# Performance work log

Hardware: AMD Instinct MI355X
Metric: run time of the kernel (lower is better)

Reference implementation:

```python
import jax, jax.numpy as jnp
import numpy as np

EMBED = 1024

def setup_inputs() -> dict:
    key = jax.random.key(0)
    ks = jax.random.split(key, 7)
    s = 1.0 / np.sqrt(EMBED)  # ~ torch Linear default init scale
    x = jax.random.normal(ks[0], (4, 2048, EMBED), dtype=jnp.float32)
    Wq = jax.random.uniform(ks[1], (EMBED, EMBED), jnp.float32, -s, s)
    bq = jax.random.uniform(ks[2], (EMBED,), jnp.float32, -s, s)
    Wk = jax.random.uniform(ks[3], (EMBED, EMBED), jnp.float32, -s, s)
    bk = jax.random.uniform(ks[4], (EMBED,), jnp.float32, -s, s)
    Wv = jax.random.uniform(ks[5], (EMBED, EMBED), jnp.float32, -s, s)
    bv = jax.random.uniform(ks[6], (EMBED,), jnp.float32, -s, s)
    return {"x": x, "Wq": Wq, "bq": bq, "Wk": Wk, "bk": bk, "Wv": Wv, "bv": bv}

def reference(x, Wq, bq, Wk, bk, Wv, bv):
    # torch nn.Linear: y = x @ W.T + b
    q = jnp.einsum('bse,oe->bso', x, Wq) + bq
    k = jnp.einsum('bse,oe->bso', x, Wk) + bk
    v = jnp.einsum('bse,oe->bso', x, Wv) + bv
    scale = 1.0 / jnp.sqrt(jnp.float32(x.shape[-1]))
    scores = jnp.einsum('bqd,bkd->bqk', q, k) * scale  # [B,S,S]
    weights = jax.nn.softmax(scores, axis=-1)
    return jnp.einsum('bqk,bkd->bqd', weights, v)
```

## Files before the change

kernel.cpp:

```cpp
#include <hip/hip_runtime.h>
#include <stdint.h>

#define B_   4
#define S_   2048
#define E_   1024
#define MQKV (B_ * S_)
#define LDP  2112

typedef __bf16 bf16x8 __attribute__((ext_vector_type(8)));
typedef float f32x4 __attribute__((ext_vector_type(4)));
typedef unsigned short u16;
typedef unsigned int u32;

__device__ __forceinline__ u16 f2bf(float x) {
  union { float f; u32 u; } c; c.f = x;
  u32 r = (c.u + 0x7FFFu + ((c.u >> 16) & 1u)) >> 16;
  return (u16)r;
}
__device__ __forceinline__ float bf2f(u16 h) {
  union { u32 u; float f; } c; c.u = ((u32)h) << 16;
  return c.f;
}

__global__ __launch_bounds__(256) void cvt_f32_bf16(const float* __restrict__ src,
                                                    u16* __restrict__ dst, int n4) {
  int i = blockIdx.x * blockDim.x + threadIdx.x;
  int st = gridDim.x * blockDim.x;
  for (; i < n4; i += st) {
    float4 f = reinterpret_cast<const float4*>(src)[i];
    ushort4 o;
    o.x = f2bf(f.x); o.y = f2bf(f.y); o.z = f2bf(f.z); o.w = f2bf(f.w);
    reinterpret_cast<ushort4*>(dst)[i] = o;
  }
}

__global__ __launch_bounds__(256) void cvt_w3(const float* __restrict__ wq,
                                              const float* __restrict__ wk,
                                              const float* __restrict__ wv,
                                              u16* __restrict__ dst) {
  const int per = E_ * E_ / 4;
  int i = blockIdx.x * blockDim.x + threadIdx.x;
  const int sel = i / per;
  const int r = i - sel * per;
  const float* src = sel == 0 ? wq : (sel == 1 ? wk : wv);
  float4 f = reinterpret_cast<const float4*>(src)[r];
  ushort4 o;
  o.x = f2bf(f.x); o.y = f2bf(f.y); o.z = f2bf(f.z); o.w = f2bf(f.w);
  reinterpret_cast<ushort4*>(dst)[i] = o;
}

#define GLOAD_LDS16(g, l)                                                      \
  __builtin_amdgcn_global_load_lds(                                            \
      (const __attribute__((address_space(1))) u32*)(g),                       \
      (__attribute__((address_space(3))) u32*)(l), 16, 0, 0)

template <int BN, int EPI>
__device__ __forceinline__ void gemm_body(
    const u16* __restrict__ A, const u16* __restrict__ Bt, void* __restrict__ Cv,
    const float* __restrict__ b0, const float* __restrict__ b1,
    int N, int K, float scale,
    long sA, long sB, long sC, long ldA, long ldB, long ldC, int gx, int gy) {
  constexpr int BM = 256;
  constexpr int NR = BN / 64;
  constexpr int L  = 2 + BN / 128;
  constexpr int BSLOT = BN * 32;

  __shared__ alignas(16) u16 lds[4 * BM * 32 + 4 * BSLOT];
  u16* lA = lds;
  u16* lB = lds + 4 * BM * 32;

  const int t = threadIdx.x;
  const int wv = t >> 6;
  const int ln = t & 63;
  const int wm = wv >> 2;
  const int wn = wv & 3;

  const int nwg = gridDim.x;
  int id = blockIdx.x;
  id = (id & 7) * (nwg >> 3) + (id >> 3);
  const int pz = gx * gy;
  const int z = id / pz;
  const int r2 = id - z * pz;
  const int by = r2 / gx;
  const int bx = r2 - by * gx;
  const int bm = by * BM;
  const int bn = bx * BN;

  A += (size_t)z * sA;
  Bt += (size_t)z * sB;

  const int srow = t >> 2;
  const int g0 = (t & 3) ^ ((srow >> 1) & 3);
  const u16* gA0 = A + (size_t)(bm + srow) * ldA + g0 * 8;
  const u16* gA1 = gA0 + (size_t)128 * ldA;
  const u16* gB0 = Bt + (size_t)(bn + srow) * ldB + g0 * 8;
  const u16* gB1 = gB0 + (size_t)128 * ldB;

  auto STAGE = [&](int u) {
    const int s = u & 3;
    const int ko = u * 32;
    GLOAD_LDS16(gA0 + ko, lA + s * 8192 + wv * 512);
    GLOAD_LDS16(gA1 + ko, lA + s * 8192 + 4096 + wv * 512);
    GLOAD_LDS16(gB0 + ko, lB + s * BSLOT + wv * 512);
    if constexpr (BN == 256) GLOAD_LDS16(gB1 + ko, lB + s * BSLOT + 4096 + wv * 512);
  };

  const int lrow = ln & 15;
  const int g = ln >> 4;
  const int aR = wm * 128 + lrow;
  const int aOff = aR * 32 + (g ^ ((aR >> 1) & 3)) * 8;
  const int bR = wn * (BN / 4) + lrow;
  const int bOff = bR * 32 + (g ^ ((bR >> 1) & 3)) * 8;

  f32x4 acc[8][NR] = {};
  const int T = K >> 5;

  bf16x8 afA[8], afB[8], bgA[NR], bgB[NR];

#define RD_A(DST, TILE) do { const u16* _p = lA + ((TILE) & 3) * 8192 + aOff;  \
  _Pragma("unroll") for (int _i = 0; _i < 8; ++_i)                             \
    DST[_i] = *reinterpret_cast<const bf16x8*>(_p + _i * 512); } while (0)
#define RD_B(DST, TILE) do { const u16* _p = lB + ((TILE) & 3) * BSLOT + bOff; \
  _Pragma("unroll") for (int _j = 0; _j < NR; ++_j)                            \
    DST[_j] = *reinterpret_cast<const bf16x8*>(_p + _j * 512); } while (0)
#define DO_MFMA(AF, BG) do { __builtin_amdgcn_s_setprio(1);                    \
  _Pragma("unroll") for (int _i = 0; _i < 8; ++_i)                             \
  _Pragma("unroll") for (int _j = 0; _j < NR; ++_j)                            \
    acc[_i][_j] = __builtin_amdgcn_mfma_f32_16x16x32_bf16(AF[_i], BG[_j],      \
                                                          acc[_i][_j], 0, 0, 0);\
  __builtin_amdgcn_s_setprio(0); } while (0)
#define VM_GATE(COND) do {                                                     \
  if (COND) { asm volatile("s_waitcnt vmcnt(%0)" :: "n"(L) : "memory"); }      \
  else { asm volatile("s_waitcnt vmcnt(0)" ::: "memory"); }                    \
  __builtin_amdgcn_s_barrier(); asm volatile("" ::: "memory"); } while (0)

  STAGE(0); STAGE(1); STAGE(2);
  asm volatile("s_waitcnt vmcnt(%0)" :: "n"(L) : "memory");
  __builtin_amdgcn_s_barrier();
  asm volatile("" ::: "memory");

  if constexpr (NR == 2) { RD_A(afA, 0); RD_B(bgA, 0); }
  else                   { RD_B(bgA, 0); }

  for (int tt = 0; tt < T; tt += 2) {
    if (tt + 3 < T) STAGE(tt + 3);
    if constexpr (NR == 2) { RD_A(afB, tt + 1); RD_B(bgB, tt + 1); DO_MFMA(afA, bgA); }
    else                   { RD_A(afA, tt); RD_B(bgB, tt + 1);     DO_MFMA(afA, bgA); }
    VM_GATE(tt + 3 < T);

    if (tt + 4 < T) STAGE(tt + 4);
    if constexpr (NR == 2) {
      if (tt + 2 < T) { RD_A(afA, tt + 2); RD_B(bgA, tt + 2); }
      DO_MFMA(afB, bgB);
    } else {
      RD_A(afA, tt + 1);
      if (tt + 2 < T) RD_B(bgA, tt + 2);
      DO_MFMA(afA, bgB);
    }
    VM_GATE(tt + 4 < T);
  }
#undef RD_A
#undef RD_B
#undef DO_MFMA
#undef VM_GATE

  const int r0 = (ln >> 4) * 4;
  const int c0 = ln & 15;
#pragma unroll
  for (int i = 0; i < 8; ++i) {
#pragma unroll
    for (int j = 0; j < NR; ++j) {
      const int col = bn + wn * (BN / 4) + j * 16 + c0;
#pragma unroll
      for (int ii = 0; ii < 4; ++ii) {
        const int row = bm + wm * 128 + i * 16 + r0 + ii;
        float v = acc[i][j][ii];
        if constexpr (EPI == 0) {
          const int sel = col >> 10;
          const int cc = col & 1023;
          const float bb = sel == 0 ? b0[cc] : b1[cc];
          ((u16*)Cv)[(size_t)sel * 8388608 + (size_t)row * 1024 + cc] = f2bf(v + bb);
        } else if constexpr (EPI == 1) {
          ((u16*)Cv)[(size_t)z * sC + (size_t)row * ldC + col] = f2bf(v + b0[row]);
        } else if constexpr (EPI == 2) {
          ((u16*)Cv)[(size_t)z * sC + (size_t)row * ldC + col] = f2bf(__expf(v * scale));
        } else {
          ((float*)Cv)[(size_t)z * sC + (size_t)row * ldC + col] = v * b0[z * 2048 + row];
        }
      }
    }
  }
}

__global__ __launch_bounds__(512, 2) void qkproj_k(
    const u16* __restrict__ A, const u16* __restrict__ Bt, void* __restrict__ Cv,
    const float* __restrict__ b0, const float* __restrict__ b1,
    int N, int K, float scale, long sA, long sB, long sC,
    long ldA, long ldB, long ldC, int gx, int gy) {
  gemm_body<256, 0>(A, Bt, Cv, b0, b1, N, K, scale, sA, sB, sC, ldA, ldB, ldC, gx, gy);
}
__global__ __launch_bounds__(512, 2) void vproj_k(
    const u16* __restrict__ A, const u16* __restrict__ Bt, void* __restrict__ Cv,
    const float* __restrict__ b0, const float* __restrict__ b1,
    int N, int K, float scale, long sA, long sB, long sC,
    long ldA, long ldB, long ldC, int gx, int gy) {
  gemm_body<128, 1>(A, Bt, Cv, b0, b1, N, K, scale, sA, sB, sC, ldA, ldB, ldC, gx, gy);
}
__global__ __launch_bounds__(512, 2) void qkt_k(
    const u16* __restrict__ A, const u16* __restrict__ Bt, void* __restrict__ Cv,
    const float* __restrict__ b0, const float* __restrict__ b1,
    int N, int K, float scale, long sA, long sB, long sC,
    long ldA, long ldB, long ldC, int gx, int gy) {
  gemm_body<256, 2>(A, Bt, Cv, b0, b1, N, K, scale, sA, sB, sC, ldA, ldB, ldC, gx, gy);
}
__global__ __launch_bounds__(512, 2) void pv_k(
    const u16* __restrict__ A, const u16* __restrict__ Bt, void* __restrict__ Cv,
    const float* __restrict__ b0, const float* __restrict__ b1,
    int N, int K, float scale, long sA, long sB, long sC,
    long ldA, long ldB, long ldC, int gx, int gy) {
  gemm_body<128, 3>(A, Bt, Cv, b0, b1, N, K, scale, sA, sB, sC, ldA, ldB, ldC, gx, gy);
}

__global__ __launch_bounds__(256) void row_invsum(const u16* __restrict__ P,
                                                  float* __restrict__ invL) {
  const int row = blockIdx.x * 4 + (threadIdx.x >> 6);
  const int ln = threadIdx.x & 63;
  const u16* p = P + (size_t)row * LDP + ln * 32;
  float s = 0.f;
#pragma unroll
  for (int q = 0; q < 4; ++q) {
    uint4 r = reinterpret_cast<const uint4*>(p)[q];
    u32 w[4] = {r.x, r.y, r.z, r.w};
#pragma unroll
    for (int k = 0; k < 4; ++k) {
      s += bf2f((u16)(w[k] & 0xffffu));
      s += bf2f((u16)(w[k] >> 16));
    }
  }
  for (int o = 1; o < 64; o <<= 1) s += __shfl_xor(s, o);
  if (ln == 0) invL[row] = 1.0f / s;
}

extern "C" void kernel_launch(void* const* d_in, const int* in_sizes, int n_in,
                              void* d_out, int out_size, void* d_ws, size_t ws_size,
                              hipStream_t stream) {
  const float* x = (const float*)d_in[0];
  const float* Wq = (const float*)d_in[1];
  const float* bq = (const float*)d_in[2];
  const float* Wk = (const float*)d_in[3];
  const float* bk = (const float*)d_in[4];
  const float* Wv = (const float*)d_in[5];
  const float* bv = (const float*)d_in[6];
  float* out = (float*)d_out;

  const size_t xE = 8388608, wE = 3145728, qE = 8388608;
  const size_t vtE = (size_t)4 * 1024 * LDP;
  const size_t PmE = (size_t)4 * 2048 * LDP;
  const size_t need = (xE + wE + 2 * qE + vtE + PmE) * 2 + (size_t)MQKV * 4;
  if (ws_size < need) {
    hipMemsetAsync(d_out, 0, (size_t)out_size * sizeof(float), stream);
    return;
  }
  u16* xb = (u16*)d_ws;
  u16* wqkv = xb + xE;
  u16* qb = wqkv + wE;
  u16* vt = qb + 2 * qE;
  u16* Pm = vt + vtE;
  float* invL = (float*)(Pm + PmE);

  cvt_f32_bf16<<<2048, 256, 0, stream>>>(x, xb, MQKV * E_ / 4);
  cvt_w3<<<3 * E_ * E_ / 4 / 256, 256, 0, stream>>>(Wq, Wk, Wv, wqkv);

  qkproj_k<<<256, 512, 0, stream>>>(
      xb, wqkv, qb, bq, bk, 2048, E_, 1.f,
      0, 0, 0, E_, E_, 1024, 8, 32);

  vproj_k<<<256, 512, 0, stream>>>(
      wqkv + 2 * (size_t)E_ * E_, xb, vt, bv, nullptr, 2048, E_, 1.f,
      0, (long)S_ * E_, (long)1024 * LDP, E_, E_, LDP, 16, 4);

  qkt_k<<<256, 512, 0, stream>>>(
      qb, qb + 8388608, Pm, nullptr, nullptr, 2048, E_, 0.03125f,
      (long)S_ * 1024, (long)S_ * 1024, (long)2048 * LDP, 1024, 1024, LDP, 8, 8);

  row_invsum<<<B_ * S_ / 4, 256, 0, stream>>>(Pm, invL);

  pv_k<<<256, 512, 0, stream>>>(
      Pm, vt, out, invL, nullptr, E_, S_, 1.f,
      (long)2048 * LDP, (long)1024 * LDP, (long)S_ * E_, LDP, LDP, 1024, 8, 8);
}
```

Baseline: 157.8 us.

## Fuse softmax row sums into QK^T epilogue and add dedicated PV kernel

The QK^T epilogue now accumulates each row's exp sum with shuffles and atomics into a zeroed buffer, which removes the separate row_invsum pass over the probability matrix. The two conversion kernels become one launch that also zeroes that buffer. PV gets its own kernel with a 3-stage LDS pipeline, 64-wide K steps and XOR swizzling, and the normalization is applied in its epilogue. This trades one launch and a full re-read of P for atomic traffic and a new, hand-scheduled GEMM loop.

```diff
diff --git a/kernel.cpp b/kernel.cpp
--- a/kernel.cpp
+++ b/kernel.cpp
@@ -17,36 +17,30 @@
   u32 r = (c.u + 0x7FFFu + ((c.u >> 16) & 1u)) >> 16;
   return (u16)r;
 }
-__device__ __forceinline__ float bf2f(u16 h) {
-  union { u32 u; float f; } c; c.u = ((u32)h) << 16;
-  return c.f;
-}
-
-__global__ __launch_bounds__(256) void cvt_f32_bf16(const float* __restrict__ src,
-                                                    u16* __restrict__ dst, int n4) {
-  int i = blockIdx.x * blockDim.x + threadIdx.x;
-  int st = gridDim.x * blockDim.x;
-  for (; i < n4; i += st) {
-    float4 f = reinterpret_cast<const float4*>(src)[i];
+
+__global__ __launch_bounds__(256) void cvt_all(
+    const float* __restrict__ x, const float* __restrict__ wq,
+    const float* __restrict__ wk, const float* __restrict__ wv,
+    u16* __restrict__ dst, float* __restrict__ Ls) {
+  const int gid = blockIdx.x * 256 + threadIdx.x;
+  if (gid < MQKV) Ls[gid] = 0.f;
+  const int total = 2097152 + 786432;
+  const int stride = gridDim.x * 256;
+  for (int i = gid; i < total; i += stride) {
+    float4 f;
+    if (i < 2097152) {
+      f = reinterpret_cast<const float4*>(x)[i];
+    } else {
+      const int j = i - 2097152;
+      const int sel = j >> 18;
+      const int r = j & 262143;
+      const float* s = sel == 0 ? wq : (sel == 1 ? wk : wv);
+      f = reinterpret_cast<const float4*>(s)[r];
+    }
     ushort4 o;
     o.x = f2bf(f.x); o.y = f2bf(f.y); o.z = f2bf(f.z); o.w = f2bf(f.w);
     reinterpret_cast<ushort4*>(dst)[i] = o;
   }
-}
-
-__global__ __launch_bounds__(256) void cvt_w3(const float* __restrict__ wq,
-                                              const float* __restrict__ wk,
-                                              const float* __restrict__ wv,
-                                              u16* __restrict__ dst) {
-  const int per = E_ * E_ / 4;
-  int i = blockIdx.x * blockDim.x + threadIdx.x;
-  const int sel = i / per;
-  const int r = i - sel * per;
-  const float* src = sel == 0 ? wq : (sel == 1 ? wk : wv);
-  float4 f = reinterpret_cast<const float4*>(src)[r];
-  ushort4 o;
-  o.x = f2bf(f.x); o.y = f2bf(f.y); o.z = f2bf(f.z); o.w = f2bf(f.w);
-  reinterpret_cast<ushort4*>(dst)[i] = o;
 }
 
 #define GLOAD_LDS16(g, l)                                                      \
@@ -57,7 +51,7 @@
 template <int BN, int EPI>
 __device__ __forceinline__ void gemm_body(
     const u16* __restrict__ A, const u16* __restrict__ Bt, void* __restrict__ Cv,
-    const float* __restrict__ b0, const float* __restrict__ b1,
+    const float* __restrict__ b0, const float* __restrict__ b1, float* __restrict__ Ls,
     int N, int K, float scale,
     long sA, long sB, long sC, long ldA, long ldB, long ldC, int gx, int gy) {
   constexpr int BM = 256;
@@ -166,26 +160,43 @@
 
   const int r0 = (ln >> 4) * 4;
   const int c0 = ln & 15;
-#pragma unroll
-  for (int i = 0; i < 8; ++i) {
-#pragma unroll
-    for (int j = 0; j < NR; ++j) {
-      const int col = bn + wn * (BN / 4) + j * 16 + c0;
+  if constexpr (EPI == 2) {
+#pragma unroll
+    for (int i = 0; i < 8; ++i) {
 #pragma unroll
       for (int ii = 0; ii < 4; ++ii) {
         const int row = bm + wm * 128 + i * 16 + r0 + ii;
-        float v = acc[i][j][ii];
-        if constexpr (EPI == 0) {
-          const int sel = col >> 10;
-          const int cc = col & 1023;
-          const float bb = sel == 0 ? b0[cc] : b1[cc];
-          ((u16*)Cv)[(size_t)sel * 8388608 + (size_t)row * 1024 + cc] = f2bf(v + bb);
-        } else if constexpr (EPI == 1) {
-          ((u16*)Cv)[(size_t)z * sC + (size_t)row * ldC + col] = f2bf(v + b0[row]);
-        } else if constexpr (EPI == 2) {
-          ((u16*)Cv)[(size_t)z * sC + (size_t)row * ldC + col] = f2bf(__expf(v * scale));
-        } else {
-          ((float*)Cv)[(size_t)z * sC + (size_t)row * ldC + col] = v * b0[z * 2048 + row];
+        float s = 0.f;
+#pragma unroll
+        for (int j = 0; j < NR; ++j) {
+          const int col = bn + wn * (BN / 4) + j * 16 + c0;
+          const float vex = __expf(acc[i][j][ii] * scale);
+          ((u16*)Cv)[(size_t)z * sC + (size_t)row * ldC + col] = f2bf(vex);
+          s += vex;
+        }
+        s += __shfl_xor(s, 1); s += __shfl_xor(s, 2);
+        s += __shfl_xor(s, 4); s += __shfl_xor(s, 8);
+        if ((ln & 15) == 0) unsafeAtomicAdd(&Ls[z * 2048 + row], s);
+      }
+    }
+  } else {
+#pragma unroll
+    for (int i = 0; i < 8; ++i) {
+#pragma unroll
+      for (int j = 0; j < NR; ++j) {
+        const int col = bn + wn * (BN / 4) + j * 16 + c0;
+#pragma unroll
+        for (int ii = 0; ii < 4; ++ii) {
+          const int row = bm + wm * 128 + i * 16 + r0 + ii;
+          float v = acc[i][j][ii];
+          if constexpr (EPI == 0) {
+            const int sel = col >> 10;
+            const int cc = col & 1023;
+            const float bb = sel == 0 ? b0[cc] : b1[cc];
+            ((u16*)Cv)[(size_t)sel * 8388608 + (size_t)row * 1024 + cc] = f2bf(v + bb);
+          } else {
+            ((u16*)Cv)[(size_t)z * sC + (size_t)row * ldC + col] = f2bf(v + b0[row]);
+          }
         }
       }
     }
@@ -197,48 +208,116 @@
     const float* __restrict__ b0, const float* __restrict__ b1,
     int N, int K, float scale, long sA, long sB, long sC,
     long ldA, long ldB, long ldC, int gx, int gy) {
-  gemm_body<256, 0>(A, Bt, Cv, b0, b1, N, K, scale, sA, sB, sC, ldA, ldB, ldC, gx, gy);
+  gemm_body<256, 0>(A, Bt, Cv, b0, b1, nullptr, N, K, scale, sA, sB, sC, ldA, ldB, ldC, gx, gy);
 }
 __global__ __launch_bounds__(512, 2) void vproj_k(
     const u16* __restrict__ A, const u16* __restrict__ Bt, void* __restrict__ Cv,
     const float* __restrict__ b0, const float* __restrict__ b1,
     int N, int K, float scale, long sA, long sB, long sC,
     long ldA, long ldB, long ldC, int gx, int gy) {
-  gemm_body<128, 1>(A, Bt, Cv, b0, b1, N, K, scale, sA, sB, sC, ldA, ldB, ldC, gx, gy);
+  gemm_body<128, 1>(A, Bt, Cv, b0, b1, nullptr, N, K, scale, sA, sB, sC, ldA, ldB, ldC, gx, gy);
 }
 __global__ __launch_bounds__(512, 2) void qkt_k(
     const u16* __restrict__ A, const u16* __restrict__ Bt, void* __restrict__ Cv,
-    const float* __restrict__ b0, const float* __restrict__ b1,
+    float* __restrict__ Ls,
     int N, int K, float scale, long sA, long sB, long sC,
     long ldA, long ldB, long ldC, int gx, int gy) {
-  gemm_body<256, 2>(A, Bt, Cv, b0, b1, N, K, scale, sA, sB, sC, ldA, ldB, ldC, gx, gy);
-}
+  gemm_body<256, 2>(A, Bt, Cv, nullptr, nullptr, Ls, N, K, scale, sA, sB, sC, ldA, ldB, ldC, gx, gy);
+}
+
 __global__ __launch_bounds__(512, 2) void pv_k(
-    const u16* __restrict__ A, const u16* __restrict__ Bt, void* __restrict__ Cv,
-    const float* __restrict__ b0, const float* __restrict__ b1,
-    int N, int K, float scale, long sA, long sB, long sC,
-    long ldA, long ldB, long ldC, int gx, int gy) {
-  gemm_body<128, 3>(A, Bt, Cv, b0, b1, N, K, scale, sA, sB, sC, ldA, ldB, ldC, gx, gy);
-}
-
-__global__ __launch_bounds__(256) void row_invsum(const u16* __restrict__ P,
-                                                  float* __restrict__ invL) {
-  const int row = blockIdx.x * 4 + (threadIdx.x >> 6);
-  const int ln = threadIdx.x & 63;
-  const u16* p = P + (size_t)row * LDP + ln * 32;
-  float s = 0.f;
-#pragma unroll
-  for (int q = 0; q < 4; ++q) {
-    uint4 r = reinterpret_cast<const uint4*>(p)[q];
-    u32 w[4] = {r.x, r.y, r.z, r.w};
-#pragma unroll
-    for (int k = 0; k < 4; ++k) {
-      s += bf2f((u16)(w[k] & 0xffffu));
-      s += bf2f((u16)(w[k] >> 16));
-    }
-  }
-  for (int o = 1; o < 64; o <<= 1) s += __shfl_xor(s, o);
-  if (ln == 0) invL[row] = 1.0f / s;
+    const u16* __restrict__ Pm, const u16* __restrict__ vt,
+    float* __restrict__ out, const float* __restrict__ Ls) {
+  __shared__ alignas(16) u16 lA[3 * 16384];
+  __shared__ alignas(16) u16 lB[3 * 8192];
+  const int t = threadIdx.x;
+  const int wv = t >> 6, ln = t & 63;
+  const int wm = wv >> 2, wn = wv & 3;
+
+  int id = blockIdx.x;
+  id = (id & 7) * 32 + (id >> 3);
+  const int z = id >> 6;
+  const int r2 = id & 63;
+  const int by = r2 >> 3, bx = r2 & 7;
+  const int bm = by * 256, bn = bx * 128;
+
+  const u16* A = Pm + (size_t)z * 2048 * LDP;
+  const u16* Bt = vt + (size_t)z * 1024 * LDP;
+
+  const int sr = t >> 3;
+  const int scw = ((t & 7) ^ (sr & 7)) * 8;
+  const u16* Ab = A + (size_t)(bm + sr) * LDP + scw;
+  const u16* Bb = Bt + (size_t)(bn + sr) * LDP + scw;
+
+#define PSTG(u) do { const int _s = (u) % 3; const long _ko = (long)(u) * 64;  \
+  _Pragma("unroll") for (int _q = 0; _q < 4; ++_q)                             \
+    GLOAD_LDS16(Ab + (size_t)_q * 64 * LDP + _ko, lA + _s * 16384 + _q * 4096 + t * 8); \
+  _Pragma("unroll") for (int _q = 0; _q < 2; ++_q)                             \
+    GLOAD_LDS16(Bb + (size_t)_q * 64 * LDP + _ko, lB + _s * 8192 + _q * 4096 + t * 8);  \
+} while (0)
+
+  const int lrow = ln & 15, g = ln >> 4;
+  const int ch0 = (g ^ (lrow & 7)) * 8;
+  const int ch1 = ((4 | g) ^ (lrow & 7)) * 8;
+
+  f32x4 acc[8][2] = {};
+
+  PSTG(0); PSTG(1);
+  asm volatile("s_waitcnt vmcnt(6)" ::: "memory");
+  __builtin_amdgcn_s_barrier();
+  asm volatile("" ::: "memory");
+
+  for (int u = 0; u < 32; ++u) {
+    if (u + 2 < 32) PSTG(u + 2);
+    const int s = u % 3;
+    const u16* pA = lA + s * 16384 + lrow * 64;
+    const u16* pB = lB + s * 8192 + lrow * 64;
+    bf16x8 a[8][2], b[2][2];
+#pragma unroll
+    for (int mf = 0; mf < 8; ++mf) {
+      const int ro = (wm * 128 + mf * 16) * 64;
+      a[mf][0] = *reinterpret_cast<const bf16x8*>(pA + ro + ch0);
+      a[mf][1] = *reinterpret_cast<const bf16x8*>(pA + ro + ch1);
+    }
+#pragma unroll
+    for (int nf = 0; nf < 2; ++nf) {
+      const int ro = (wn * 32 + nf * 16) * 64;
+      b[nf][0] = *reinterpret_cast<const bf16x8*>(pB + ro + ch0);
+      b[nf][1] = *reinterpret_cast<const bf16x8*>(pB + ro + ch1);
+    }
+    __builtin_amdgcn_s_setprio(1);
+#pragma unroll
+    for (int ks = 0; ks < 2; ++ks)
+#pragma unroll
+      for (int mf = 0; mf < 8; ++mf)
+#pragma unroll
+        for (int nf = 0; nf < 2; ++nf)
+          acc[mf][nf] = __builtin_amdgcn_mfma_f32_16x16x32_bf16(
+              a[mf][ks], b[nf][ks], acc[mf][nf], 0, 0, 0);
+    __builtin_amdgcn_s_setprio(0);
+    if (u < 31) {
+      if (u + 2 < 32) { asm volatile("s_waitcnt vmcnt(6)" ::: "memory"); }
+      else            { asm volatile("s_waitcnt vmcnt(0)" ::: "memory"); }
+      __builtin_amdgcn_s_barrier();
+      asm volatile("" ::: "memory");
+    }
+  }
+#undef PSTG
+
+  const int r0 = g * 4, c0 = lrow;
+#pragma unroll
+  for (int mf = 0; mf < 8; ++mf) {
+#pragma unroll
+    for (int ii = 0; ii < 4; ++ii) {
+      const int row = bm + wm * 128 + mf * 16 + r0 + ii;
+      const float inv = 1.0f / Ls[z * 2048 + row];
+#pragma unroll
+      for (int nf = 0; nf < 2; ++nf) {
+        const int col = bn + wn * 32 + nf * 16 + c0;
+        out[((size_t)z * 2048 + row) * 1024 + col] = acc[mf][nf][ii] * inv;
+      }
+    }
+  }
 }
 
 extern "C" void kernel_launch(void* const* d_in, const int* in_sizes, int n_in,
@@ -266,10 +345,9 @@
   u16* qb = wqkv + wE;
   u16* vt = qb + 2 * qE;
   u16* Pm = vt + vtE;
-  float* invL = (float*)(Pm + PmE);
-
-  cvt_f32_bf16<<<2048, 256, 0, stream>>>(x, xb, MQKV * E_ / 4);
-  cvt_w3<<<3 * E_ * E_ / 4 / 256, 256, 0, stream>>>(Wq, Wk, Wv, wqkv);
+  float* Ls = (float*)(Pm + PmE);
+
+  cvt_all<<<2048, 256, 0, stream>>>(x, Wq, Wk, Wv, xb, Ls);
 
   qkproj_k<<<256, 512, 0, stream>>>(
       xb, wqkv, qb, bq, bk, 2048, E_, 1.f,
@@ -280,12 +358,8 @@
       0, (long)S_ * E_, (long)1024 * LDP, E_, E_, LDP, 16, 4);
 
   qkt_k<<<256, 512, 0, stream>>>(
-      qb, qb + 8388608, Pm, nullptr, nullptr, 2048, E_, 0.03125f,
+      qb, qb + 8388608, Pm, Ls, 2048, E_, 0.03125f,
       (long)S_ * 1024, (long)S_ * 1024, (long)2048 * LDP, 1024, 1024, LDP, 8, 8);
 
-  row_invsum<<<B_ * S_ / 4, 256, 0, stream>>>(Pm, invL);
-
-  pv_k<<<256, 512, 0, stream>>>(
-      Pm, vt, out, invL, nullptr, E_, S_, 1.f,
-      (long)2048 * LDP, (long)1024 * LDP, (long)S_ * E_, LDP, LDP, 1024, 8, 8);
-}
+  pv_k<<<256, 512, 0, stream>>>(Pm, vt, out, Ls);
+}
```

Result: no change. 160.3 us (+1.6%).

## Fuse softmax row-sum into PV GEMM and merge conversion kernels

Applied to the files above, without the earlier changes.

Removes the separate row_invsum kernel by accumulating row sums of the exponentiated scores from the A fragments already loaded into registers inside a dedicated PV GEMM, then reducing them across lanes and normalizing in the epilogue via LDS. Also merges the x and weight fp32-to-bf16 conversions into one grid-stride kernel. This saves one full read of the 4x2048x2112 bf16 P matrix and two launches, at the cost of extra VALU work (bf16 unpack and add) inside the MFMA main loop and a hand-specialized copy of the GEMM pipeline.

```diff
diff --git a/kernel.cpp b/kernel.cpp
--- a/kernel.cpp
+++ b/kernel.cpp
@@ -22,31 +22,28 @@
   return c.f;
 }
 
-__global__ __launch_bounds__(256) void cvt_f32_bf16(const float* __restrict__ src,
-                                                    u16* __restrict__ dst, int n4) {
-  int i = blockIdx.x * blockDim.x + threadIdx.x;
-  int st = gridDim.x * blockDim.x;
-  for (; i < n4; i += st) {
-    float4 f = reinterpret_cast<const float4*>(src)[i];
+__global__ __launch_bounds__(256) void cvt_all(
+    const float* __restrict__ x, const float* __restrict__ wq,
+    const float* __restrict__ wk, const float* __restrict__ wv,
+    u16* __restrict__ dst) {
+  const int gid = blockIdx.x * 256 + threadIdx.x;
+  const int total = 2097152 + 786432;
+  const int stride = gridDim.x * 256;
+  for (int i = gid; i < total; i += stride) {
+    float4 f;
+    if (i < 2097152) {
+      f = reinterpret_cast<const float4*>(x)[i];
+    } else {
+      const int j = i - 2097152;
+      const int sel = j >> 18;
+      const int r = j & 262143;
+      const float* s = sel == 0 ? wq : (sel == 1 ? wk : wv);
+      f = reinterpret_cast<const float4*>(s)[r];
+    }
     ushort4 o;
     o.x = f2bf(f.x); o.y = f2bf(f.y); o.z = f2bf(f.z); o.w = f2bf(f.w);
     reinterpret_cast<ushort4*>(dst)[i] = o;
   }
-}
-
-__global__ __launch_bounds__(256) void cvt_w3(const float* __restrict__ wq,
-                                              const float* __restrict__ wk,
-                                              const float* __restrict__ wv,
-                                              u16* __restrict__ dst) {
-  const int per = E_ * E_ / 4;
-  int i = blockIdx.x * blockDim.x + threadIdx.x;
-  const int sel = i / per;
-  const int r = i - sel * per;
-  const float* src = sel == 0 ? wq : (sel == 1 ? wk : wv);
-  float4 f = reinterpret_cast<const float4*>(src)[r];
-  ushort4 o;
-  o.x = f2bf(f.x); o.y = f2bf(f.y); o.z = f2bf(f.z); o.w = f2bf(f.w);
-  reinterpret_cast<ushort4*>(dst)[i] = o;
 }
 
 #define GLOAD_LDS16(g, l)                                                      \
@@ -182,10 +179,8 @@
           ((u16*)Cv)[(size_t)sel * 8388608 + (size_t)row * 1024 + cc] = f2bf(v + bb);
         } else if constexpr (EPI == 1) {
           ((u16*)Cv)[(size_t)z * sC + (size_t)row * ldC + col] = f2bf(v + b0[row]);
-        } else if constexpr (EPI == 2) {
+        } else {
           ((u16*)Cv)[(size_t)z * sC + (size_t)row * ldC + col] = f2bf(__expf(v * scale));
-        } else {
-          ((float*)Cv)[(size_t)z * sC + (size_t)row * ldC + col] = v * b0[z * 2048 + row];
         }
       }
     }
@@ -213,32 +208,133 @@
     long ldA, long ldB, long ldC, int gx, int gy) {
   gemm_body<256, 2>(A, Bt, Cv, b0, b1, N, K, scale, sA, sB, sC, ldA, ldB, ldC, gx, gy);
 }
+
 __global__ __launch_bounds__(512, 2) void pv_k(
-    const u16* __restrict__ A, const u16* __restrict__ Bt, void* __restrict__ Cv,
-    const float* __restrict__ b0, const float* __restrict__ b1,
-    int N, int K, float scale, long sA, long sB, long sC,
-    long ldA, long ldB, long ldC, int gx, int gy) {
-  gemm_body<128, 3>(A, Bt, Cv, b0, b1, N, K, scale, sA, sB, sC, ldA, ldB, ldC, gx, gy);
-}
-
-__global__ __launch_bounds__(256) void row_invsum(const u16* __restrict__ P,
-                                                  float* __restrict__ invL) {
-  const int row = blockIdx.x * 4 + (threadIdx.x >> 6);
-  const int ln = threadIdx.x & 63;
-  const u16* p = P + (size_t)row * LDP + ln * 32;
-  float s = 0.f;
-#pragma unroll
-  for (int q = 0; q < 4; ++q) {
-    uint4 r = reinterpret_cast<const uint4*>(p)[q];
-    u32 w[4] = {r.x, r.y, r.z, r.w};
-#pragma unroll
-    for (int k = 0; k < 4; ++k) {
-      s += bf2f((u16)(w[k] & 0xffffu));
-      s += bf2f((u16)(w[k] >> 16));
-    }
-  }
-  for (int o = 1; o < 64; o <<= 1) s += __shfl_xor(s, o);
-  if (ln == 0) invL[row] = 1.0f / s;
+    const u16* __restrict__ Pm, const u16* __restrict__ vt,
+    float* __restrict__ out) {
+  constexpr int BN = 128, BM = 256, NR = 2, L = 3, BSLOT = BN * 32;
+  __shared__ alignas(16) u16 lds[4 * BM * 32 + 4 * BSLOT];
+  u16* lA = lds;
+  u16* lB = lds + 4 * BM * 32;
+
+  const int t = threadIdx.x;
+  const int wv = t >> 6, ln = t & 63;
+  const int wm = wv >> 2, wn = wv & 3;
+
+  int id = blockIdx.x;
+  id = (id & 7) * 32 + (id >> 3);
+  const int z = id >> 6;
+  const int r2 = id & 63;
+  const int by = r2 >> 3, bx = r2 & 7;
+  const int bm = by * 256, bn = bx * 128;
+
+  const u16* A = Pm + (size_t)z * 2048 * LDP;
+  const u16* Bt = vt + (size_t)z * 1024 * LDP;
+
+  const int srow = t >> 2;
+  const int g0 = (t & 3) ^ ((srow >> 1) & 3);
+  const u16* gA0 = A + (size_t)(bm + srow) * LDP + g0 * 8;
+  const u16* gA1 = gA0 + (size_t)128 * LDP;
+  const u16* gB0 = Bt + (size_t)(bn + srow) * LDP + g0 * 8;
+
+  auto STAGE = [&](int u) {
+    const int s = u & 3;
+    const int ko = u * 32;
+    GLOAD_LDS16(gA0 + ko, lA + s * 8192 + wv * 512);
+    GLOAD_LDS16(gA1 + ko, lA + s * 8192 + 4096 + wv * 512);
+    GLOAD_LDS16(gB0 + ko, lB + s * BSLOT + wv * 512);
+  };
+
+  const int lrow = ln & 15;
+  const int g = ln >> 4;
+  const int aR = wm * 128 + lrow;
+  const int aOff = aR * 32 + (g ^ ((aR >> 1) & 3)) * 8;
+  const int bR = wn * (BN / 4) + lrow;
+  const int bOff = bR * 32 + (g ^ ((bR >> 1) & 3)) * 8;
+
+  f32x4 acc[8][NR] = {};
+  float rs[8] = {};
+  const int T = 64;
+
+  bf16x8 afA[8], afB[8], bgA[NR], bgB[NR];
+
+  auto ACCRS = [&](bf16x8* AF) {
+#pragma unroll
+    for (int i = 0; i < 8; ++i) {
+      const u32* w = reinterpret_cast<const u32*>(&AF[i]);
+#pragma unroll
+      for (int q = 0; q < 4; ++q)
+        rs[i] += bf2f((u16)(w[q] & 0xffffu)) + bf2f((u16)(w[q] >> 16));
+    }
+  };
+
+#define RD_A(DST, TILE) do { const u16* _p = lA + ((TILE) & 3) * 8192 + aOff;  \
+  _Pragma("unroll") for (int _i = 0; _i < 8; ++_i)                             \
+    DST[_i] = *reinterpret_cast<const bf16x8*>(_p + _i * 512); } while (0)
+#define RD_B(DST, TILE) do { const u16* _p = lB + ((TILE) & 3) * BSLOT + bOff; \
+  _Pragma("unroll") for (int _j = 0; _j < NR; ++_j)                            \
+    DST[_j] = *reinterpret_cast<const bf16x8*>(_p + _j * 512); } while (0)
+#define DO_MFMA(AF, BG) do { __builtin_amdgcn_s_setprio(1);                    \
+  _Pragma("unroll") for (int _i = 0; _i < 8; ++_i)                             \
+  _Pragma("unroll") for (int _j = 0; _j < NR; ++_j)                            \
+    acc[_i][_j] = __builtin_amdgcn_mfma_f32_16x16x32_bf16(AF[_i], BG[_j],      \
+                                                          acc[_i][_j], 0, 0, 0);\
+  __builtin_amdgcn_s_setprio(0); } while (0)
+#define VM_GATE(COND) do {                                                     \
+  if (COND) { asm volatile("s_waitcnt vmcnt(%0)" :: "n"(L) : "memory"); }      \
+  else { asm volatile("s_waitcnt vmcnt(0)" ::: "memory"); }                    \
+  __builtin_amdgcn_s_barrier(); asm volatile("" ::: "memory"); } while (0)
+
+  STAGE(0); STAGE(1); STAGE(2);
+  asm volatile("s_waitcnt vmcnt(%0)" :: "n"(L) : "memory");
+  __builtin_amdgcn_s_barrier();
+  asm volatile("" ::: "memory");
+
+  RD_A(afA, 0); RD_B(bgA, 0);
+
+  for (int tt = 0; tt < T; tt += 2) {
+    if (tt + 3 < T) STAGE(tt + 3);
+    RD_A(afB, tt + 1); RD_B(bgB, tt + 1);
+    DO_MFMA(afA, bgA);
+    ACCRS(afA);
+    VM_GATE(tt + 3 < T);
+
+    if (tt + 4 < T) STAGE(tt + 4);
+    if (tt + 2 < T) { RD_A(afA, tt + 2); RD_B(bgA, tt + 2); }
+    DO_MFMA(afB, bgB);
+    ACCRS(afB);
+    VM_GATE(tt + 4 < T);
+  }
+#undef RD_A
+#undef RD_B
+#undef DO_MFMA
+#undef VM_GATE
+
+  __syncthreads();
+  float* sums = reinterpret_cast<float*>(lds);
+#pragma unroll
+  for (int i = 0; i < 8; ++i) {
+    float s = rs[i];
+    s += __shfl_xor(s, 16);
+    s += __shfl_xor(s, 32);
+    if (wn == 0 && g == 0) sums[wm * 128 + i * 16 + lrow] = s;
+  }
+  __syncthreads();
+
+  const int r0 = g * 4, c0 = lrow;
+#pragma unroll
+  for (int i = 0; i < 8; ++i) {
+#pragma unroll
+    for (int ii = 0; ii < 4; ++ii) {
+      const int lr = wm * 128 + i * 16 + r0 + ii;
+      const float inv = 1.0f / sums[lr];
+#pragma unroll
+      for (int j = 0; j < NR; ++j) {
+        const int col = bn + wn * 32 + j * 16 + c0;
+        out[((size_t)z * 2048 + bm + lr) * 1024 + col] = acc[i][j][ii] * inv;
+      }
+    }
+  }
 }
 
 extern "C" void kernel_launch(void* const* d_in, const int* in_sizes, int n_in,
@@ -256,7 +352,7 @@
   const size_t xE = 8388608, wE = 3145728, qE = 8388608;
   const size_t vtE = (size_t)4 * 1024 * LDP;
   const size_t PmE = (size_t)4 * 2048 * LDP;
-  const size_t need = (xE + wE + 2 * qE + vtE + PmE) * 2 + (size_t)MQKV * 4;
+  const size_t need = (xE + wE + 2 * qE + vtE + PmE) * 2;
   if (ws_size < need) {
     hipMemsetAsync(d_out, 0, (size_t)out_size * sizeof(float), stream);
     return;
@@ -266,10 +362,8 @@
   u16* qb = wqkv + wE;
   u16* vt = qb + 2 * qE;
   u16* Pm = vt + vtE;
-  float* invL = (float*)(Pm + PmE);
-
-  cvt_f32_bf16<<<2048, 256, 0, stream>>>(x, xb, MQKV * E_ / 4);
-  cvt_w3<<<3 * E_ * E_ / 4 / 256, 256, 0, stream>>>(Wq, Wk, Wv, wqkv);
+
+  cvt_all<<<2048, 256, 0, stream>>>(x, Wq, Wk, Wv, xb);
 
   qkproj_k<<<256, 512, 0, stream>>>(
       xb, wqkv, qb, bq, bk, 2048, E_, 1.f,
@@ -283,9 +377,5 @@
       qb, qb + 8388608, Pm, nullptr, nullptr, 2048, E_, 0.03125f,
       (long)S_ * 1024, (long)S_ * 1024, (long)2048 * LDP, 1024, 1024, LDP, 8, 8);
 
-  row_invsum<<<B_ * S_ / 4, 256, 0, stream>>>(Pm, invL);
-
-  pv_k<<<256, 512, 0, stream>>>(
-      Pm, vt, out, invL, nullptr, E_, S_, 1.f,
-      (long)2048 * LDP, (long)1024 * LDP, (long)S_ * E_, LDP, LDP, 1024, 8, 8);
-}
+  pv_k<<<256, 512, 0, stream>>>(Pm, vt, out);
+}
```

New measurement: 166.5 us. 5.5% more time.
